# Kernel tuning notes

Hardware: AMD Instinct MI355X
Metric: run time of the kernel (lower is better)

The kernel has to match this reference:

```python
import jax, jax.numpy as jnp
import numpy as np

# dims: batch, encoder frames, encoder dim, pred-net hidden, joint dim, vocab (blank = V)
B, T, ENC, H, J, V = 32, 64, 1024, 320, 320, 1024
BLANK = V
MAXSYM = 2            # max_symbols_per_step
S = T * MAXSYM        # upper bound on loop-labels iterations (<= MAXSYM steps per frame due to force-blank)


def setup_inputs() -> dict:
    key = jax.random.key(0)
    ks = jax.random.split(key, 10)
    s = 0.05
    return {
        "x": jax.random.normal(ks[0], (B, T, ENC), jnp.float32),
        "out_len": jax.random.randint(ks[1], (B,), T // 2, T + 1, dtype=jnp.int32),
        "W_enc": jax.random.normal(ks[2], (ENC, J), jnp.float32) * s,
        "b_enc": jnp.zeros((J,), jnp.float32),
        "Emb": jax.random.normal(ks[3], (V, H), jnp.float32) * s,
        "W_ih": jax.random.normal(ks[4], (H, 4 * H), jnp.float32) * s,
        "W_hh": jax.random.normal(ks[5], (H, 4 * H), jnp.float32) * s,
        "b_lstm": jnp.zeros((4 * H,), jnp.float32),
        "W_pred": jax.random.normal(ks[6], (H, J), jnp.float32) * s,
        "b_pred": jnp.zeros((J,), jnp.float32),
        "W_out": jax.random.normal(ks[7], (J, V + 1), jnp.float32) * s,
        "b_out": jnp.zeros((V + 1,), jnp.float32),
    }


def _lstm_step(emb, h, c, W_ih, W_hh, b):
    g = emb @ W_ih + h @ W_hh + b
    i, f, gg, o = jnp.split(g, 4, axis=-1)
    c2 = jax.nn.sigmoid(f) * c + jax.nn.sigmoid(i) * jnp.tanh(gg)
    h2 = jax.nn.sigmoid(o) * jnp.tanh(c2)
    return h2, c2


def reference(x, out_len, W_enc, b_enc, Emb, W_ih, W_hh, b_lstm, W_pred, b_pred, W_out, b_out):
    # project_encoder once (as in the torch module)
    x_proj = x @ W_enc + b_enc                      # [B, T, J]
    # SOS step: zero embedding, zero LSTM state (decoder.predict(None, None))
    z = jnp.zeros((B, H), x.dtype)
    h0, c0 = _lstm_step(z, z, z, W_ih, W_hh, b_lstm)
    dec0 = h0 @ W_pred + b_pred                     # project_prednet

    def step(carry, _):
        time, symbols, h, c, dec = carry
        enc_t = jnp.take_along_axis(x_proj, time[:, None, None].astype(jnp.int32), axis=1)[:, 0]  # [B, J]
        logits = jax.nn.relu(enc_t + dec) @ W_out + b_out  # joint_after_projection, [B, V+1]
        scores = logits.max(-1)
        labels = jnp.argmax(logits, -1)
        active = time < out_len
        emit = active & (labels != BLANK)
        # prediction-network step for elements that emitted a non-blank label
        emb = Emb[jnp.where(emit, labels, 0)]
        h2, c2 = _lstm_step(emb, h, c, W_ih, W_hh, b_lstm)
        dec2 = h2 @ W_pred + b_pred
        m = emit[:, None]
        h = jnp.where(m, h2, h)
        c = jnp.where(m, c2, c)
        dec = jnp.where(m, dec2, dec)
        sym2 = jnp.where(emit, symbols + 1, jnp.zeros_like(symbols))
        force = emit & (sym2 >= MAXSYM)             # force blank after max_symbols on one frame
        advance = (active & ~emit) | force          # blank (or forced blank) advances time
        time2 = time + advance.astype(time.dtype)
        sym2 = jnp.where(advance, jnp.zeros_like(sym2), sym2)
        out = (jnp.where(emit, labels, BLANK).astype(jnp.int32),
               jnp.where(active, scores, jnp.zeros_like(scores)),
               time.astype(jnp.int32),
               emit)
        return (time2, sym2, h, c, dec), out

    init = (jnp.zeros((B,), jnp.int32), jnp.zeros((B,), jnp.int32), h0, c0, dec0)
    _, (lab, sc, tm, em) = jax.lax.scan(step, init, None, length=S)
    lengths = em.astype(jnp.int32).sum(0)
    # lab/sc/tm: [S, B] alignment-style records (BLANK filler when nothing emitted);
    # lengths: number of emitted (non-blank) labels per utterance -> equals batched_hyps contents.
    return lab, sc, tm, lengths
```

## Files before the change

### kernel.cpp

```cpp
#include <hip/hip_runtime.h>
#include <math.h>

typedef unsigned long long ull;

constexpr int Bn = 32, Tn = 64, Hn = 320, Jn = 320, Vn = 1024, Sn = 128;
constexpr int G4n = 1280, VP1 = 1025, WO4S = 1028;

constexpr int OFF_XP  = 0;
constexpr int OFF_G   = OFF_XP + Bn*Tn*Jn;
constexpr int OFF_WO4 = OFF_G + Vn*G4n;
constexpr int OFF_WH4 = OFF_WO4 + 80*WO4S*4;
constexpr int OFF_WP4 = OFF_WH4 + 80*G4n*4;
constexpr int OFF_CB  = OFF_WP4 + 80*Jn*4;
constexpr int OFF_DEC = OFF_CB + 2*Bn*Hn;
constexpr int OFF_GB  = OFF_DEC + 2*Bn*Jn;
constexpr int OFF_PB  = OFF_GB + 2*Bn*G4n;
constexpr int OFF_REC = OFF_PB + 2*Bn*8*1028;

__device__ __forceinline__ float sigmf(float x) { return 1.0f / (1.0f + expf(-x)); }

__device__ __forceinline__ ull pack_key(float v, int idx) {
    unsigned u = __float_as_uint(v);
    u = (u & 0x80000000u) ? ~u : (u | 0x80000000u);
    return ((ull)u << 32) | (unsigned)(0x7FFFFFFF - idx);
}
__device__ __forceinline__ float key_val(ull k) {
    unsigned u = (unsigned)(k >> 32);
    return __uint_as_float((u & 0x80000000u) ? (u & 0x7FFFFFFFu) : ~u);
}
__device__ __forceinline__ int key_idx(ull k) { return 0x7FFFFFFF - (int)(k & 0xFFFFFFFFu); }

__device__ __forceinline__ void gemm_tile(const float* __restrict__ A,
                                          const float* __restrict__ Bm,
                                          const float* __restrict__ bias,
                                          float* __restrict__ C,
                                          int M, int N, int K, int bx, int by,
                                          float (*As)[68], float (*Bs)[65]) {
    const int tx = threadIdx.x & 15, ty = threadIdx.x >> 4;
    const int n0 = bx * 64, m0 = by * 64;
    float acc[4][4] = {};
    for (int k0 = 0; k0 < K; k0 += 16) {
        for (int i = threadIdx.x; i < 1024; i += 256) {
            int mm = i >> 4, kk = i & 15;
            As[kk][mm] = A[(m0 + mm) * K + k0 + kk];
            int kk2 = i >> 6, nn = i & 63;
            Bs[kk2][nn] = Bm[(k0 + kk2) * N + n0 + nn];
        }
        __syncthreads();
#pragma unroll
        for (int kk = 0; kk < 16; ++kk) {
            float av[4], bv[4];
#pragma unroll
            for (int r = 0; r < 4; ++r) { av[r] = As[kk][ty * 4 + r]; bv[r] = Bs[kk][tx * 4 + r]; }
#pragma unroll
            for (int i2 = 0; i2 < 4; ++i2)
#pragma unroll
                for (int j2 = 0; j2 < 4; ++j2) acc[i2][j2] += av[i2] * bv[j2];
        }
        __syncthreads();
    }
#pragma unroll
    for (int i2 = 0; i2 < 4; ++i2)
#pragma unroll
        for (int j2 = 0; j2 < 4; ++j2)
            C[(m0 + ty * 4 + i2) * N + n0 + tx * 4 + j2] = acc[i2][j2] + bias[n0 + tx * 4 + j2];
}

__global__ __launch_bounds__(256) void preamble(
    const float* __restrict__ x, const float* __restrict__ W_enc,
    const float* __restrict__ b_enc, const float* __restrict__ Emb,
    const float* __restrict__ W_ih, const float* __restrict__ b_lstm,
    const float* __restrict__ W_hh, const float* __restrict__ W_pred,
    const float* __restrict__ W_out,
    float* __restrict__ xp, float* __restrict__ Gm,
    float* __restrict__ Wo4, float* __restrict__ Wh4, float* __restrict__ Wp4) {
    __shared__ float As[16][68];
    __shared__ float Bs[16][65];
    const int blk = blockIdx.x;
    if (blk < 160) {
        gemm_tile(x, W_enc, b_enc, xp, Bn * Tn, Jn, 1024, blk % 5, blk / 5, As, Bs);
    } else if (blk < 480) {
        const int t = blk - 160;
        gemm_tile(Emb, W_ih, b_lstm, Gm, Vn, G4n, Hn, t % 20, t / 20, As, Bs);
    } else if (blk < 560) {
        const int k4 = blk - 480;
        for (int c = threadIdx.x; c < VP1; c += 256) {
            float4 v;
            v.x = W_out[(k4 * 4 + 0) * VP1 + c];
            v.y = W_out[(k4 * 4 + 1) * VP1 + c];
            v.z = W_out[(k4 * 4 + 2) * VP1 + c];
            v.w = W_out[(k4 * 4 + 3) * VP1 + c];
            ((float4*)Wo4)[(size_t)k4 * WO4S + c] = v;
        }
    } else if (blk < 640) {
        const int k4 = blk - 560;
        for (int c = threadIdx.x; c < G4n; c += 256) {
            float4 v;
            v.x = W_hh[(k4 * 4 + 0) * G4n + c];
            v.y = W_hh[(k4 * 4 + 1) * G4n + c];
            v.z = W_hh[(k4 * 4 + 2) * G4n + c];
            v.w = W_hh[(k4 * 4 + 3) * G4n + c];
            ((float4*)Wh4)[(size_t)k4 * G4n + c] = v;
        }
    } else {
        const int k4 = blk - 640;
        for (int c = threadIdx.x; c < Jn; c += 256) {
            float4 v;
            v.x = W_pred[(k4 * 4 + 0) * Jn + c];
            v.y = W_pred[(k4 * 4 + 1) * Jn + c];
            v.z = W_pred[(k4 * 4 + 2) * Jn + c];
            v.w = W_pred[(k4 * 4 + 3) * Jn + c];
            ((float4*)Wp4)[(size_t)k4 * Jn + c] = v;
        }
    }
}

__global__ __launch_bounds__(320, 1) void rnnt_step(
    const float* __restrict__ xp, const float* __restrict__ Gm,
    const float* __restrict__ Wo4, const float* __restrict__ Wh4,
    const float* __restrict__ Wp4,
    const float* __restrict__ b_out, const float* __restrict__ b_lstm,
    const float* __restrict__ b_pred, const int* __restrict__ out_len,
    float* __restrict__ cb, float* __restrict__ db, float* __restrict__ gb,
    float* __restrict__ pb, int* __restrict__ rec, float* __restrict__ out,
    int L) {
    __shared__ __align__(16) float h_s[Hn];
    __shared__ __align__(16) float f_s[48];
    __shared__ float dec_s[40];
    __shared__ ull wk_s[5];

    const int w = blockIdx.x, tid = threadIdx.x;
    const int b = w & 31, m = w >> 5;
    const int ol = out_len[b];
    const float4* Wo4f = (const float4*)Wo4;
    const float4* Wh4f = (const float4*)Wh4;
    const float4* Wp4f = (const float4*)Wp4;
    const float4* h4 = (const float4*)h_s;

    int tnew, genN;
    bool doDec;
    if (L == 0) {
        float c0 = sigmf(b_lstm[tid]) * tanhf(b_lstm[2 * Hn + tid]);
        float h0 = sigmf(b_lstm[3 * Hn + tid]) * tanhf(c0);
        h_s[tid] = h0;
        int lc = tid - m * 40;
        if (lc >= 0 && lc < 40) cb[b * Hn + tid] = c0;
        if (m == 0 && tid == 0) {
            int* rn = rec + b * 4;
            rn[0] = 0; rn[1] = 0; rn[2] = 0;
        }
        tnew = 0; genN = 0; doDec = true;
        __syncthreads();
    } else {
        const int* rp = rec + ((L - 1) & 1) * Bn * 4 + b * 4;
        const int told = rp[0], sold = rp[1], len = rp[2];
        const float* gq = gb + (size_t)((len & 1) * Bn + b) * G4n;
        const float* cv = cb + (size_t)((len & 1) * Bn + b) * Hn;
        float g0 = gq[tid], g1 = gq[Hn + tid], g2 = gq[2 * Hn + tid], g3 = gq[3 * Hn + tid];
        float crv = cv[tid];
        asm volatile("" ::: "memory");
        const float* pp = pb + (size_t)(((L - 1) & 1) * Bn + b) * 8 * 1028;
        ull key = 0;
        for (int c = tid; c < VP1; c += 320) {
            float sv = b_out[c];
#pragma unroll
            for (int mm = 0; mm < 8; ++mm) sv += pp[mm * 1028 + c];
            ull k2 = pack_key(sv, c);
            if (k2 > key) key = k2;
        }
#pragma unroll
        for (int d = 1; d < 64; d <<= 1) {
            ull o = __shfl_xor(key, d, 64);
            if (o > key) key = o;
        }
        if ((tid & 63) == 0) wk_s[tid >> 6] = key;
        __syncthreads();
        ull bk = wk_s[0];
#pragma unroll
        for (int i = 1; i < 5; ++i) if (wk_s[i] > bk) bk = wk_s[i];
        const int label = key_idx(bk);
        const bool active = told < ol;
        const bool emit = active && (label != Vn);
        int sym2 = emit ? sold + 1 : 0;
        const bool force = emit && (sym2 >= 2);
        const bool advance = (active && !emit) || force;
        tnew = told + (advance ? 1 : 0);
        sym2 = advance ? 0 : sym2;
        const int newlen = len + (emit ? 1 : 0);
        if (m == 0 && tid == 0) {
            out[(L - 1) * Bn + b] = emit ? (float)label : 1024.0f;
            out[Sn * Bn + (L - 1) * Bn + b] = active ? key_val(bk) : 0.0f;
            out[2 * Sn * Bn + (L - 1) * Bn + b] = (float)told;
            int* rn = rec + (L & 1) * Bn * 4 + b * 4;
            rn[0] = tnew; rn[1] = sym2; rn[2] = newlen;
            if (L == Sn) out[3 * Sn * Bn + b] = (float)newlen;
        }
        if (L == Sn) return;
        if (tnew >= ol) return;
        genN = newlen;
        doDec = emit;
        if (emit) {
            const float* gE = Gm + (size_t)label * G4n;
            float xi = g0 + gE[tid];
            float xf = g1 + gE[Hn + tid];
            float xg = g2 + gE[2 * Hn + tid];
            float xo = g3 + gE[3 * Hn + tid];
            float c2 = sigmf(xf) * crv + sigmf(xi) * tanhf(xg);
            float h2 = sigmf(xo) * tanhf(c2);
            h_s[tid] = h2;
            int lc = tid - m * 40;
            if (lc >= 0 && lc < 40)
                cb[(size_t)((newlen & 1) * Bn + b) * Hn + tid] = c2;
        } else {
            if (tid < 40)
                dec_s[tid] = db[(size_t)((len & 1) * Bn + b) * Jn + m * 40 + tid];
        }
        __syncthreads();
    }
    if (doDec) {
        if (tid < 160) {
            const int c = m * 160 + tid;
            float ax = 0.f, ay = 0.f, az = 0.f, aw = 0.f;
#pragma unroll 20
            for (int k4 = 0; k4 < 80; ++k4) {
                float4 wv = Wh4f[(size_t)k4 * G4n + c];
                float4 hv = h4[k4];
                ax += wv.x * hv.x; ay += wv.y * hv.y;
                az += wv.z * hv.z; aw += wv.w * hv.w;
            }
            gb[(size_t)((genN & 1) * Bn + b) * G4n + c] = ax + ay + az + aw;
        } else if (tid < 200) {
            const int lc = tid - 160;
            const int c = m * 40 + lc;
            float ax = 0.f, ay = 0.f, az = 0.f, aw = 0.f;
#pragma unroll 20
            for (int k4 = 0; k4 < 80; ++k4) {
                float4 wv = Wp4f[(size_t)k4 * Jn + c];
                float4 hv = h4[k4];
                ax += wv.x * hv.x; ay += wv.y * hv.y;
                az += wv.z * hv.z; aw += wv.w * hv.w;
            }
            float d = b_pred[c] + ax + ay + az + aw;
            dec_s[lc] = d;
            db[(size_t)((genN & 1) * Bn + b) * Jn + c] = d;
        }
        __syncthreads();
    }
    if (tid < 40) {
        const int tc = tnew < (Tn - 1) ? tnew : (Tn - 1);
        f_s[tid] = fmaxf(xp[(size_t)(b * Tn + tc) * Jn + m * 40 + tid] + dec_s[tid], 0.0f);
    }
    __syncthreads();
    {
        const float4* f4 = (const float4*)f_s;
        float4 fr[10];
#pragma unroll
        for (int j = 0; j < 10; ++j) fr[j] = f4[j];
        float* pw = pb + (size_t)((L & 1) * Bn + b) * 8 * 1028 + m * 1028;
        for (int c = tid; c < VP1; c += 320) {
            float ax = 0.f, ay = 0.f, az = 0.f, aw = 0.f;
#pragma unroll
            for (int j = 0; j < 10; ++j) {
                float4 wv = Wo4f[(size_t)(10 * m + j) * WO4S + c];
                float4 fv = fr[j];
                ax += wv.x * fv.x; ay += wv.y * fv.y;
                az += wv.z * fv.z; aw += wv.w * fv.w;
            }
            pw[c] = ax + ay + az + aw;
        }
    }
}

extern "C" void kernel_launch(void* const* d_in, const int* in_sizes, int n_in,
                              void* d_out, int out_size, void* d_ws, size_t ws_size,
                              hipStream_t stream) {
    (void)in_sizes; (void)n_in; (void)out_size; (void)ws_size;
    const float* x      = (const float*)d_in[0];
    const int*   outlen = (const int*)d_in[1];
    const float* W_enc  = (const float*)d_in[2];
    const float* b_enc  = (const float*)d_in[3];
    const float* Emb    = (const float*)d_in[4];
    const float* W_ih   = (const float*)d_in[5];
    const float* W_hh   = (const float*)d_in[6];
    const float* b_lstm = (const float*)d_in[7];
    const float* W_pred = (const float*)d_in[8];
    const float* b_pred = (const float*)d_in[9];
    const float* W_out  = (const float*)d_in[10];
    const float* b_out  = (const float*)d_in[11];

    float* ws  = (float*)d_ws;
    float* xp  = ws + OFF_XP;
    float* Gm  = ws + OFF_G;
    float* Wo4 = ws + OFF_WO4;
    float* Wh4 = ws + OFF_WH4;
    float* Wp4 = ws + OFF_WP4;
    float* cb  = ws + OFF_CB;
    float* db  = ws + OFF_DEC;
    float* gb  = ws + OFF_GB;
    float* pb  = ws + OFF_PB;
    int*   rec = (int*)(ws + OFF_REC);

    preamble<<<720, 256, 0, stream>>>(x, W_enc, b_enc, Emb, W_ih, b_lstm,
                                      W_hh, W_pred, W_out,
                                      xp, Gm, Wo4, Wh4, Wp4);

    for (int L = 0; L <= Sn; ++L)
        rnnt_step<<<256, 320, 0, stream>>>(xp, Gm, Wo4, Wh4, Wp4,
                                           b_out, b_lstm, b_pred, outlen,
                                           cb, db, gb, pb, rec,
                                           (float*)d_out, L);
}
```

Before: 1.939 ms.

## Use 128-row GEMM tiles, early-exit finished utterances, vectorize logit partial reduction

The preamble GEMMs switch to 128x64 tiles with 8x4 register blocking, which halves the block count and raises arithmetic reuse per shared-memory load. In the per-step kernel, an utterance that is already past its length now writes its filler records and returns before loading LSTM state or reducing logits. The reduction over partial logits now reads float4 vectors with 257 threads. Together these cut preamble overhead and per-step memory traffic, at the cost of fewer preamble blocks to spread across the GPU.

After: 1.996 ms. 3.0% more time.

```diff
diff --git a/kernel.cpp b/kernel.cpp
--- a/kernel.cpp
+++ b/kernel.cpp
@@ -30,40 +30,45 @@
 }
 __device__ __forceinline__ int key_idx(ull k) { return 0x7FFFFFFF - (int)(k & 0xFFFFFFFFu); }
 
-__device__ __forceinline__ void gemm_tile(const float* __restrict__ A,
-                                          const float* __restrict__ Bm,
-                                          const float* __restrict__ bias,
-                                          float* __restrict__ C,
-                                          int M, int N, int K, int bx, int by,
-                                          float (*As)[68], float (*Bs)[65]) {
+__device__ __forceinline__ void gemm_tile128(const float* __restrict__ A,
+                                             const float* __restrict__ Bm,
+                                             const float* __restrict__ bias,
+                                             float* __restrict__ C,
+                                             int N, int K, int bx, int by,
+                                             float (*As)[132], float (*Bs)[65]) {
     const int tx = threadIdx.x & 15, ty = threadIdx.x >> 4;
-    const int n0 = bx * 64, m0 = by * 64;
-    float acc[4][4] = {};
+    const int n0 = bx * 64, m0 = by * 128;
+    float acc[8][4] = {};
     for (int k0 = 0; k0 < K; k0 += 16) {
+        for (int i = threadIdx.x; i < 2048; i += 256) {
+            int mm = i >> 4, kk = i & 15;
+            As[kk][mm] = A[(size_t)(m0 + mm) * K + k0 + kk];
+        }
         for (int i = threadIdx.x; i < 1024; i += 256) {
-            int mm = i >> 4, kk = i & 15;
-            As[kk][mm] = A[(m0 + mm) * K + k0 + kk];
             int kk2 = i >> 6, nn = i & 63;
-            Bs[kk2][nn] = Bm[(k0 + kk2) * N + n0 + nn];
+            Bs[kk2][nn] = Bm[(size_t)(k0 + kk2) * N + n0 + nn];
         }
         __syncthreads();
 #pragma unroll
         for (int kk = 0; kk < 16; ++kk) {
-            float av[4], bv[4];
-#pragma unroll
-            for (int r = 0; r < 4; ++r) { av[r] = As[kk][ty * 4 + r]; bv[r] = Bs[kk][tx * 4 + r]; }
-#pragma unroll
-            for (int i2 = 0; i2 < 4; ++i2)
+            float av[8], bv[4];
+#pragma unroll
+            for (int r = 0; r < 8; ++r) av[r] = As[kk][ty * 8 + r];
+#pragma unroll
+            for (int r = 0; r < 4; ++r) bv[r] = Bs[kk][tx * 4 + r];
+#pragma unroll
+            for (int i2 = 0; i2 < 8; ++i2)
 #pragma unroll
                 for (int j2 = 0; j2 < 4; ++j2) acc[i2][j2] += av[i2] * bv[j2];
         }
         __syncthreads();
     }
 #pragma unroll
-    for (int i2 = 0; i2 < 4; ++i2)
+    for (int i2 = 0; i2 < 8; ++i2)
 #pragma unroll
         for (int j2 = 0; j2 < 4; ++j2)
-            C[(m0 + ty * 4 + i2) * N + n0 + tx * 4 + j2] = acc[i2][j2] + bias[n0 + tx * 4 + j2];
+            C[(size_t)(m0 + ty * 8 + i2) * N + n0 + tx * 4 + j2] =
+                acc[i2][j2] + bias[n0 + tx * 4 + j2];
 }
 
 __global__ __launch_bounds__(256) void preamble(
@@ -74,16 +79,16 @@
     const float* __restrict__ W_out,
     float* __restrict__ xp, float* __restrict__ Gm,
     float* __restrict__ Wo4, float* __restrict__ Wh4, float* __restrict__ Wp4) {
-    __shared__ float As[16][68];
+    __shared__ float As[16][132];
     __shared__ float Bs[16][65];
     const int blk = blockIdx.x;
-    if (blk < 160) {
-        gemm_tile(x, W_enc, b_enc, xp, Bn * Tn, Jn, 1024, blk % 5, blk / 5, As, Bs);
-    } else if (blk < 480) {
-        const int t = blk - 160;
-        gemm_tile(Emb, W_ih, b_lstm, Gm, Vn, G4n, Hn, t % 20, t / 20, As, Bs);
-    } else if (blk < 560) {
-        const int k4 = blk - 480;
+    if (blk < 80) {
+        gemm_tile128(x, W_enc, b_enc, xp, Jn, 1024, blk % 5, blk / 5, As, Bs);
+    } else if (blk < 240) {
+        const int t = blk - 80;
+        gemm_tile128(Emb, W_ih, b_lstm, Gm, G4n, Hn, t % 20, t / 20, As, Bs);
+    } else if (blk < 320) {
+        const int k4 = blk - 240;
         for (int c = threadIdx.x; c < VP1; c += 256) {
             float4 v;
             v.x = W_out[(k4 * 4 + 0) * VP1 + c];
@@ -92,8 +97,8 @@
             v.w = W_out[(k4 * 4 + 3) * VP1 + c];
             ((float4*)Wo4)[(size_t)k4 * WO4S + c] = v;
         }
-    } else if (blk < 640) {
-        const int k4 = blk - 560;
+    } else if (blk < 400) {
+        const int k4 = blk - 320;
         for (int c = threadIdx.x; c < G4n; c += 256) {
             float4 v;
             v.x = W_hh[(k4 * 4 + 0) * G4n + c];
@@ -103,7 +108,7 @@
             ((float4*)Wh4)[(size_t)k4 * G4n + c] = v;
         }
     } else {
-        const int k4 = blk - 640;
+        const int k4 = blk - 400;
         for (int c = threadIdx.x; c < Jn; c += 256) {
             float4 v;
             v.x = W_pred[(k4 * 4 + 0) * Jn + c];
@@ -154,19 +159,36 @@
     } else {
         const int* rp = rec + ((L - 1) & 1) * Bn * 4 + b * 4;
         const int told = rp[0], sold = rp[1], len = rp[2];
+        if (told >= ol) {
+            if (m == 0 && tid == 0) {
+                out[(L - 1) * Bn + b] = 1024.0f;
+                out[Sn * Bn + (L - 1) * Bn + b] = 0.0f;
+                out[2 * Sn * Bn + (L - 1) * Bn + b] = (float)told;
+                int* rn = rec + (L & 1) * Bn * 4 + b * 4;
+                rn[0] = told; rn[1] = 0; rn[2] = len;
+                if (L == Sn) out[3 * Sn * Bn + b] = (float)len;
+            }
+            return;
+        }
         const float* gq = gb + (size_t)((len & 1) * Bn + b) * G4n;
         const float* cv = cb + (size_t)((len & 1) * Bn + b) * Hn;
         float g0 = gq[tid], g1 = gq[Hn + tid], g2 = gq[2 * Hn + tid], g3 = gq[3 * Hn + tid];
         float crv = cv[tid];
         asm volatile("" ::: "memory");
-        const float* pp = pb + (size_t)(((L - 1) & 1) * Bn + b) * 8 * 1028;
+        const float4* pp4 = (const float4*)(pb + (size_t)(((L - 1) & 1) * Bn + b) * 8 * 1028);
         ull key = 0;
-        for (int c = tid; c < VP1; c += 320) {
-            float sv = b_out[c];
-#pragma unroll
-            for (int mm = 0; mm < 8; ++mm) sv += pp[mm * 1028 + c];
-            ull k2 = pack_key(sv, c);
-            if (k2 > key) key = k2;
+        if (tid < 257) {
+            float4 sv = make_float4(0.f, 0.f, 0.f, 0.f);
+#pragma unroll
+            for (int mm = 0; mm < 8; ++mm) {
+                float4 v = pp4[mm * 257 + tid];
+                sv.x += v.x; sv.y += v.y; sv.z += v.z; sv.w += v.w;
+            }
+            const int c0 = tid * 4;
+            key = pack_key(sv.x + b_out[c0], c0);
+            if (c0 + 1 < VP1) { ull k2 = pack_key(sv.y + b_out[c0 + 1], c0 + 1); if (k2 > key) key = k2; }
+            if (c0 + 2 < VP1) { ull k2 = pack_key(sv.z + b_out[c0 + 2], c0 + 2); if (k2 > key) key = k2; }
+            if (c0 + 3 < VP1) { ull k2 = pack_key(sv.w + b_out[c0 + 3], c0 + 3); if (k2 > key) key = k2; }
         }
 #pragma unroll
         for (int d = 1; d < 64; d <<= 1) {
@@ -179,17 +201,16 @@
 #pragma unroll
         for (int i = 1; i < 5; ++i) if (wk_s[i] > bk) bk = wk_s[i];
         const int label = key_idx(bk);
-        const bool active = told < ol;
-        const bool emit = active && (label != Vn);
+        const bool emit = (label != Vn);
         int sym2 = emit ? sold + 1 : 0;
         const bool force = emit && (sym2 >= 2);
-        const bool advance = (active && !emit) || force;
+        const bool advance = (!emit) || force;
         tnew = told + (advance ? 1 : 0);
         sym2 = advance ? 0 : sym2;
         const int newlen = len + (emit ? 1 : 0);
         if (m == 0 && tid == 0) {
             out[(L - 1) * Bn + b] = emit ? (float)label : 1024.0f;
-            out[Sn * Bn + (L - 1) * Bn + b] = active ? key_val(bk) : 0.0f;
+            out[Sn * Bn + (L - 1) * Bn + b] = key_val(bk);
             out[2 * Sn * Bn + (L - 1) * Bn + b] = (float)told;
             int* rn = rec + (L & 1) * Bn * 4 + b * 4;
             rn[0] = tnew; rn[1] = sym2; rn[2] = newlen;
@@ -300,7 +321,7 @@
     float* pb  = ws + OFF_PB;
     int*   rec = (int*)(ws + OFF_REC);
 
-    preamble<<<720, 256, 0, stream>>>(x, W_enc, b_enc, Emb, W_ih, b_lstm,
+    preamble<<<480, 256, 0, stream>>>(x, W_enc, b_enc, Emb, W_ih, b_lstm,
                                       W_hh, W_pred, W_out,
                                       xp, Gm, Wo4, Wh4, Wp4);
 
```
